# Kernel tuning notes

Hardware: AMD Instinct MI355X
Metric: run time of the kernel (lower is better)

## Reference

```python
import jax, jax.numpy as jnp
import numpy as np

B, M, R = 32, 64, 8  # batch, n_comps+1, n_rel_types+1


def setup_inputs() -> dict:
    key = jax.random.key(0)
    k1, k2 = jax.random.split(key)
    log_energies = jax.random.normal(k1, (B, M, M, R), dtype=jnp.float32)
    label_tree = jax.random.randint(k2, (B, M, 3), 0, R, dtype=jnp.int32)
    return {"log_energies": log_energies, "label_tree": label_tree}


def _mst_single(le):
    """Greedy (Kruskal-style) MST on one [M, M, R] energy tensor.
    Returns (mst_energy scalar, edges [M, 3] int)."""
    m = le.shape[0]

    def step(carry, _):
        mst_e, le, parts = carry  # parts: [M, M] bool partition membership
        flat = jnp.argmax(le)
        i, j, k = jnp.unravel_index(flat, le.shape)
        max_e = le[i, j, k]
        upd = jnp.logical_not(jnp.isneginf(max_e))
        mst_e = mst_e + jnp.where(upd, max_e, 0.0)
        link = jnp.where(upd, jnp.stack([i, j, k]).astype(jnp.int32), 0)
        mf = parts[i]  # [M] members of i's partition
        mt = parts[j]  # [M] members of j's partition
        # Forbid all edges (both directions) between the two merged partitions.
        block = mf[:, None] & mt[None, :]
        block = block | block.T
        le = jnp.where(block[:, :, None], -jnp.inf, le)
        # Merge partitions: every node in the union gets the union row.
        merged = mf | mt
        parts = jnp.where(merged[:, None], merged[None, :], parts)
        return (mst_e, le, parts), link

    init = (jnp.float32(0.0), le, jnp.eye(m, dtype=bool))
    (mst_e, _, _), edges = jax.lax.scan(step, init, None, length=m)
    return mst_e, edges


def _score_single(le, tree):
    # (0,0,0) entry is zeroed so padded (0,0,0) edges contribute nothing.
    le = le.at[0, 0, 0].set(0.0)
    return jnp.sum(le[tree[:, 0], tree[:, 1], tree[:, 2]])


def reference(log_energies, label_tree):
    """disc_loss: mean(MST energy - label tree score) over the batch."""
    mst_energies, _ = jax.vmap(_mst_single)(log_energies)          # [B]
    label_scores = jax.vmap(_score_single)(log_energies, label_tree)  # [B]
    return jnp.mean(mst_energies - label_scores)
```

## Files before the change

### kernel.cpp

```cpp
#include <hip/hip_runtime.h>
#include <math.h>

#define BATCH 32
#define M 64
#define R 8
typedef unsigned long long u64;
typedef unsigned int u32;

#define SWZ_SLOT(r, s) ((s) ^ ((r) & 7))
#define PM_IDX(r, c) ((((r) << 6)) + ((SWZ_SLOT((r), (c) >> 2) << 2) | ((c) & 3)))

#define NSLOT 33

__device__ __forceinline__ u32 umax2(u32 a, u32 b) { return a > b ? a : b; }
__device__ __forceinline__ u32 umax3(u32 a, u32 b, u32 c) {
    return umax2(umax2(a, b), c);
}

__device__ __forceinline__ u32 sortable(float f) {
    const u32 u = __float_as_uint(f);
    return u ^ ((u32)(((int)u) >> 31) | 0x80000000u);
}
__device__ __forceinline__ float unsortable(u32 k) {
    const u32 fb = (k & 0x80000000u) ? (k ^ 0x80000000u) : ~k;
    return __uint_as_float(fb);
}

#define SEXTBIT(w, j) ((u32)(((int)((w) << (31 - (j)))) >> 31))

__device__ __forceinline__ u32 wave_umax_scalar(u32 g) {
    int v = (int)g;
    const int s1a = __builtin_amdgcn_update_dpp(v, v, 0x111, 0xf, 0xf, false);
    const int s1b = __builtin_amdgcn_update_dpp(v, v, 0x112, 0xf, 0xf, false);
    const u32 t1 = umax3(g, (u32)s1a, (u32)s1b);
    const int w = (int)t1;
    const int s2a = __builtin_amdgcn_update_dpp(w, w, 0x113, 0xf, 0xf, false);
    const int s2b = __builtin_amdgcn_update_dpp(w, w, 0x116, 0xf, 0xf, false);
    const u32 t2 = umax3(t1, (u32)s2a, (u32)s2b);
    const int y = (int)t2;
    const int s3 = __builtin_amdgcn_update_dpp(y, y, 0x117, 0xf, 0xf, false);
    const u32 t3 = umax2(t2, (u32)s3);
    const u32 a = (u32)__builtin_amdgcn_readlane((int)t3, 15);
    const u32 b = (u32)__builtin_amdgcn_readlane((int)t3, 31);
    const u32 c = (u32)__builtin_amdgcn_readlane((int)t3, 47);
    const u32 d = (u32)__builtin_amdgcn_readlane((int)t3, 63);
    return umax2(umax2(a, b), umax2(c, d));
}

__device__ __forceinline__ u64 readlane_u64(u64 v, int lane) {
    unsigned lo = (unsigned)__builtin_amdgcn_readlane((int)(unsigned)v, lane);
    unsigned hi = (unsigned)__builtin_amdgcn_readlane((int)(v >> 32), lane);
    return ((u64)hi << 32) | lo;
}

#define KM(j) (q##j & SEXTBIT(cmb, j))
#define T1G(n, A, B, C2) const u32 a##n = umax3(KM(A), KM(B), KM(C2));
#define LOADK(k) const u32 q##k = fold_lds[fbase + (k)];

__global__ __launch_bounds__(256)
__attribute__((amdgpu_waves_per_eu(1, 1)))
void tree_crf_mst_kernel(const float* __restrict__ le,
                         const int* __restrict__ tree,
                         float* __restrict__ mst_out,
                         float* __restrict__ ls_out)
{
    __shared__ __align__(16) float pm[M * M];
    __shared__ u32 fold_lds[M * NSLOT];
    const int b = blockIdx.x;
    const int tt = threadIdx.x;
    const float* bl = le + (size_t)b * M * M * R;
    const float4* g4 = reinterpret_cast<const float4*>(bl);

    for (int q = tt; q < M * M; q += 256) {
        const float4 a  = g4[2 * q];
        const float4 c4 = g4[2 * q + 1];
        const float mx = fmaxf(fmaxf(fmaxf(a.x, a.y), fmaxf(a.z, a.w)),
                               fmaxf(fmaxf(c4.x, c4.y), fmaxf(c4.z, c4.w)));
        const int rr = q >> 6, cc = q & 63;
        pm[PM_IDX(rr, cc)] = mx;
    }
    __syncthreads();

    for (int S = tt; S < M * NSLOT; S += 256) {
        const int k = S >> 6, lane = S & 63;
        const int s = lane >> 1, e = lane & 1;
        int r, c; bool valid = true;
        if (k == 32)      { r = lane; c = lane; }
        else if (!e)      { r = 63 - s; c = k; }
        else if (k <= 30 - s) { r = 63 - s; c = 32 + k; }
        else if (k <= 30) { r = s; c = k - (31 - s); }
        else              { r = 0; c = 0; valid = false; }
        u32 key = 0;
        if (valid) {
            const u32 v = umax2(sortable(pm[PM_IDX(r, c)]),
                                sortable(pm[PM_IDX(c, r)]));
            key = (v & 0xFFFFF000u) | ((u32)(63 - r) << 6) | (u32)(63 - c);
        }
        fold_lds[lane * NSLOT + k] = key;
    }
    __syncthreads();

    const int wave = tt >> 6;
    const int t = tt & 63;

    if (wave == 1) {
        const int* tr = tree + ((size_t)b * M + t) * 3;
        const int i0 = tr[0], i1 = tr[1], i2 = tr[2];
        float ls = 0.0f;
        if (!((i0 == 0) & (i1 == 0) & (i2 == 0)))
            ls = bl[(size_t)((i0 << 6) | i1) * R + i2];
        #pragma unroll
        for (int off = 32; off; off >>= 1) ls += __shfl_down(ls, off);
        if (t == 0) ls_out[b] = ls;
        return;
    }
    if (wave != 0) return;

    const int fbase = t * NSLOT;
    LOADK(0)  LOADK(1)  LOADK(2)  LOADK(3)  LOADK(4)  LOADK(5)
    LOADK(6)  LOADK(7)  LOADK(8)  LOADK(9)  LOADK(10) LOADK(11)
    LOADK(12) LOADK(13) LOADK(14) LOADK(15) LOADK(16) LOADK(17)
    LOADK(18) LOADK(19) LOADK(20) LOADK(21) LOADK(22) LOADK(23)
    LOADK(24) LOADK(25) LOADK(26) LOADK(27) LOADK(28) LOADK(29)
    LOADK(30) LOADK(31) LOADK(32)

    const int s  = t >> 1;
    const int eO = t & 1;
    const int rB = 63 - s, rA = s;
    const int shA = 31 - s, shC = s + 1;
    const u64 lanebit = 1ull << t;

    u64 mask = lanebit;
    u32 nBlo = 0xFFFFFFFFu, nBhi = 0xFFFFFFFFu;
    u32 nA   = 0xFFFFFFFFu;
    u32 dm   = 0xFFFFFFFFu;
    float mst = 0.0f;

    #pragma unroll 1
    for (int it = 0; it < M; ++it) {
        const u32 cmbO = ((nBhi << shC) >> shC) | (nA << shA);
        const u32 cmb  = eO ? cmbO : nBlo;

        T1G(0,0,1,2)    T1G(1,3,4,5)    T1G(2,6,7,8)    T1G(3,9,10,11)
        T1G(4,12,13,14) T1G(5,15,16,17) T1G(6,18,19,20) T1G(7,21,22,23)
        T1G(8,24,25,26) T1G(9,27,28,29)
        const u32 a10 = umax3(KM(30), KM(31), q32 & dm);
        const u32 b0 = umax3(a0, a1, a2);
        const u32 b1 = umax3(a3, a4, a5);
        const u32 b2 = umax3(a6, a7, a8);
        const u32 b3 = umax2(a9, a10);
        const u32 rowmax = umax3(umax2(b0, b1), b2, b3);

        const u32 gv = wave_umax_scalar(rowmax);
        const int gi = 63 - (int)((gv >> 6) & 63u);
        const int gj = 63 - (int)(gv & 63u);
        const u64 mf = readlane_u64(mask, gi);
        const u64 mt = readlane_u64(mask, gj);

        mst += unsortable((gv & 0xFFFFF000u) | 0x800u);

        const u64 merged = mf | mt;
        if (merged & lanebit) mask = merged;

        const u64 rbB = (((u32)(mf >> rB) & 1u) ? mt : 0ull) |
                        (((u32)(mt >> rB) & 1u) ? mf : 0ull);
        nBlo &= ~(u32)rbB;
        nBhi &= ~(u32)(rbB >> 32);
        const u32 rbA = (((u32)(mf >> rA) & 1u) ? (u32)mt : 0u) |
                        (((u32)(mt >> rA) & 1u) ? (u32)mf : 0u);
        nA &= ~rbA;
        dm &= ~(0u - ((u32)(mf >> t) & (u32)(mt >> t) & 1u));
    }
    if (t == 0) mst_out[b] = mst;
}

__global__ void tree_crf_reduce_kernel(const float* __restrict__ mst_p,
                                       const float* __restrict__ ls_p,
                                       float* __restrict__ out)
{
    if (threadIdx.x == 0 && blockIdx.x == 0) {
        float s = 0.0f;
        for (int i = 0; i < BATCH; ++i) s += mst_p[i] - ls_p[i];
        out[0] = s * (1.0f / BATCH);
    }
}

extern "C" void kernel_launch(void* const* d_in, const int* in_sizes, int n_in,
                              void* d_out, int out_size, void* d_ws, size_t ws_size,
                              hipStream_t stream) {
    const float* le   = (const float*)d_in[0];
    const int*   tree = (const int*)d_in[1];
    float* out = (float*)d_out;
    float* mst_p = (float*)d_ws;
    float* ls_p  = mst_p + BATCH;

    tree_crf_mst_kernel<<<BATCH, 256, 0, stream>>>(le, tree, mst_p, ls_p);
    tree_crf_reduce_kernel<<<1, 64, 0, stream>>>(mst_p, ls_p, out);
}
```

Baseline: 35.45 us.

## Fuse batch reduction into MST kernel via atomicAdd and simplify alive-slot masking

Removes the separate single-thread reduce kernel: each block now combines its MST energy and label score through shared memory and atomically adds its share of the mean into the output, with a memset to zero it first. The per-iteration mask bookkeeping is also restructured so a single 'alive' bitmask is updated directly from the kill slots, instead of rebuilding a combined mask from three partial masks each iteration. The diagonal mask update is done only when gi==gj. This trades a kernel launch for a memset plus float atomics, which makes the summation order nondeterministic.

```diff
diff --git a/kernel.cpp b/kernel.cpp
--- a/kernel.cpp
+++ b/kernel.cpp
@@ -53,7 +53,7 @@
     return ((u64)hi << 32) | lo;
 }
 
-#define KM(j) (q##j & SEXTBIT(cmb, j))
+#define KM(j) (q##j & SEXTBIT(alive, j))
 #define T1G(n, A, B, C2) const u32 a##n = umax3(KM(A), KM(B), KM(C2));
 #define LOADK(k) const u32 q##k = fold_lds[fbase + (k)];
 
@@ -61,11 +61,11 @@
 __attribute__((amdgpu_waves_per_eu(1, 1)))
 void tree_crf_mst_kernel(const float* __restrict__ le,
                          const int* __restrict__ tree,
-                         float* __restrict__ mst_out,
-                         float* __restrict__ ls_out)
+                         float* __restrict__ out)
 {
     __shared__ __align__(16) float pm[M * M];
     __shared__ u32 fold_lds[M * NSLOT];
+    __shared__ float ls_sh;
     const int b = blockIdx.x;
     const int tt = threadIdx.x;
     const float* bl = le + (size_t)b * M * M * R;
@@ -102,6 +102,7 @@
 
     const int wave = tt >> 6;
     const int t = tt & 63;
+    float mst = 0.0f;
 
     if (wave == 1) {
         const int* tr = tree + ((size_t)b * M + t) * 3;
@@ -111,78 +112,70 @@
             ls = bl[(size_t)((i0 << 6) | i1) * R + i2];
         #pragma unroll
         for (int off = 32; off; off >>= 1) ls += __shfl_down(ls, off);
-        if (t == 0) ls_out[b] = ls;
-        return;
+        if (t == 0) ls_sh = ls;
     }
-    if (wave != 0) return;
 
-    const int fbase = t * NSLOT;
-    LOADK(0)  LOADK(1)  LOADK(2)  LOADK(3)  LOADK(4)  LOADK(5)
-    LOADK(6)  LOADK(7)  LOADK(8)  LOADK(9)  LOADK(10) LOADK(11)
-    LOADK(12) LOADK(13) LOADK(14) LOADK(15) LOADK(16) LOADK(17)
-    LOADK(18) LOADK(19) LOADK(20) LOADK(21) LOADK(22) LOADK(23)
-    LOADK(24) LOADK(25) LOADK(26) LOADK(27) LOADK(28) LOADK(29)
-    LOADK(30) LOADK(31) LOADK(32)
+    if (wave == 0) {
+        const int fbase = t * NSLOT;
+        LOADK(0)  LOADK(1)  LOADK(2)  LOADK(3)  LOADK(4)  LOADK(5)
+        LOADK(6)  LOADK(7)  LOADK(8)  LOADK(9)  LOADK(10) LOADK(11)
+        LOADK(12) LOADK(13) LOADK(14) LOADK(15) LOADK(16) LOADK(17)
+        LOADK(18) LOADK(19) LOADK(20) LOADK(21) LOADK(22) LOADK(23)
+        LOADK(24) LOADK(25) LOADK(26) LOADK(27) LOADK(28) LOADK(29)
+        LOADK(30) LOADK(31) LOADK(32)
 
-    const int s  = t >> 1;
-    const int eO = t & 1;
-    const int rB = 63 - s, rA = s;
-    const int shA = 31 - s, shC = s + 1;
-    const u64 lanebit = 1ull << t;
+        const int s  = t >> 1;
+        const int eO = t & 1;
+        const int rB = 63 - s, rA = s;
+        const int shA = 31 - s;
+        const u32 maskC = (1u << (31 - s)) - 1u;
+        const u32 maskA = (1u << s) - 1u;
+        const u64 lanebit = 1ull << t;
 
-    u64 mask = lanebit;
-    u32 nBlo = 0xFFFFFFFFu, nBhi = 0xFFFFFFFFu;
-    u32 nA   = 0xFFFFFFFFu;
-    u32 dm   = 0xFFFFFFFFu;
-    float mst = 0.0f;
+        u64 mask = lanebit;
+        u32 alive = 0xFFFFFFFFu;
+        u32 dmask = 0xFFFFFFFFu;
 
-    #pragma unroll 1
-    for (int it = 0; it < M; ++it) {
-        const u32 cmbO = ((nBhi << shC) >> shC) | (nA << shA);
-        const u32 cmb  = eO ? cmbO : nBlo;
+        #pragma unroll 1
+        for (int it = 0; it < M; ++it) {
+            T1G(0,0,1,2)    T1G(1,3,4,5)    T1G(2,6,7,8)    T1G(3,9,10,11)
+            T1G(4,12,13,14) T1G(5,15,16,17) T1G(6,18,19,20) T1G(7,21,22,23)
+            T1G(8,24,25,26) T1G(9,27,28,29)
+            const u32 a10 = umax3(KM(30), KM(31), q32 & dmask);
+            const u32 b0 = umax3(a0, a1, a2);
+            const u32 b1 = umax3(a3, a4, a5);
+            const u32 b2 = umax3(a6, a7, a8);
+            const u32 b3 = umax2(a9, a10);
+            const u32 rowmax = umax3(umax2(b0, b1), b2, b3);
 
-        T1G(0,0,1,2)    T1G(1,3,4,5)    T1G(2,6,7,8)    T1G(3,9,10,11)
-        T1G(4,12,13,14) T1G(5,15,16,17) T1G(6,18,19,20) T1G(7,21,22,23)
-        T1G(8,24,25,26) T1G(9,27,28,29)
-        const u32 a10 = umax3(KM(30), KM(31), q32 & dm);
-        const u32 b0 = umax3(a0, a1, a2);
-        const u32 b1 = umax3(a3, a4, a5);
-        const u32 b2 = umax3(a6, a7, a8);
-        const u32 b3 = umax2(a9, a10);
-        const u32 rowmax = umax3(umax2(b0, b1), b2, b3);
+            const u32 gv = wave_umax_scalar(rowmax);
+            const int gi = 63 - (int)((gv >> 6) & 63u);
+            const int gj = 63 - (int)(gv & 63u);
+            const u64 mf = readlane_u64(mask, gi);
+            const u64 mt = readlane_u64(mask, gj);
 
-        const u32 gv = wave_umax_scalar(rowmax);
-        const int gi = 63 - (int)((gv >> 6) & 63u);
-        const int gj = 63 - (int)(gv & 63u);
-        const u64 mf = readlane_u64(mask, gi);
-        const u64 mt = readlane_u64(mask, gj);
+            const u32 bBP = (u32)(mf >> rB) & 1u, bBQ = (u32)(mt >> rB) & 1u;
+            const u64 rbB = (bBP ? mt : 0ull) | (bBQ ? mf : 0ull);
+            const u32 bAP = (u32)(mf >> rA) & 1u, bAQ = (u32)(mt >> rA) & 1u;
+            const u32 rbA = (bAP ? (u32)mt : 0u) | (bAQ ? (u32)mf : 0u);
+            const u32 kOdd = (((u32)(rbB >> 32)) & maskC) |
+                             ((rbA & maskA) << shA);
+            const u32 kslots = eO ? kOdd : (u32)rbB;
+            alive &= ~kslots;
+            if (gi == gj) {
+                const u32 inP = (u32)(mf >> t) & 1u;
+                dmask &= (inP - 1u);
+            }
 
-        mst += unsortable((gv & 0xFFFFF000u) | 0x800u);
+            mst += unsortable((gv & 0xFFFFF000u) | 0x800u);
+            const u64 merged = mf | mt;
+            if (merged & lanebit) mask = merged;
+        }
+    }
 
-        const u64 merged = mf | mt;
-        if (merged & lanebit) mask = merged;
-
-        const u64 rbB = (((u32)(mf >> rB) & 1u) ? mt : 0ull) |
-                        (((u32)(mt >> rB) & 1u) ? mf : 0ull);
-        nBlo &= ~(u32)rbB;
-        nBhi &= ~(u32)(rbB >> 32);
-        const u32 rbA = (((u32)(mf >> rA) & 1u) ? (u32)mt : 0u) |
-                        (((u32)(mt >> rA) & 1u) ? (u32)mf : 0u);
-        nA &= ~rbA;
-        dm &= ~(0u - ((u32)(mf >> t) & (u32)(mt >> t) & 1u));
-    }
-    if (t == 0) mst_out[b] = mst;
-}
-
-__global__ void tree_crf_reduce_kernel(const float* __restrict__ mst_p,
-                                       const float* __restrict__ ls_p,
-                                       float* __restrict__ out)
-{
-    if (threadIdx.x == 0 && blockIdx.x == 0) {
-        float s = 0.0f;
-        for (int i = 0; i < BATCH; ++i) s += mst_p[i] - ls_p[i];
-        out[0] = s * (1.0f / BATCH);
-    }
+    __syncthreads();
+    if (wave == 0 && t == 0)
+        atomicAdd(out, (mst - ls_sh) * (1.0f / BATCH));
 }
 
 extern "C" void kernel_launch(void* const* d_in, const int* in_sizes, int n_in,
@@ -191,9 +184,7 @@
     const float* le   = (const float*)d_in[0];
     const int*   tree = (const int*)d_in[1];
     float* out = (float*)d_out;
-    float* mst_p = (float*)d_ws;
-    float* ls_p  = mst_p + BATCH;
 
-    tree_crf_mst_kernel<<<BATCH, 256, 0, stream>>>(le, tree, mst_p, ls_p);
-    tree_crf_reduce_kernel<<<1, 64, 0, stream>>>(mst_p, ls_p, out);
+    hipMemsetAsync(out, 0, sizeof(float), stream);
+    tree_crf_mst_kernel<<<BATCH, 256, 0, stream>>>(le, tree, out);
 }
```

Result: slower. 40.29 us (+13.6%).
